# Optimization experiments

Hardware: AMD Instinct MI355X
Metric: run time of the kernel (lower is better)

## Reference

```python
import jax, jax.numpy as jnp
import numpy as np

L, H, N = 8192, 1024, 1024
MAX_PHASE = 6.283


def setup_inputs() -> dict:
    key = jax.random.key(0)
    ks = jax.random.split(key, 9)
    input_real = jax.random.uniform(ks[0], (L, H), dtype=jnp.float32)
    input_imag = jax.random.uniform(ks[1], (L, H), dtype=jnp.float32)
    # LRU parameter init (r_min=0, r_max=1, max_phase=6.283)
    u1 = jax.random.uniform(ks[2], (N,), dtype=jnp.float32)
    u2 = jax.random.uniform(ks[3], (N,), dtype=jnp.float32)
    nu_log = jnp.log(-0.5 * jnp.log(u1))
    theta_log = jnp.log(u2 * MAX_PHASE)
    B_real = jax.random.normal(ks[4], (N, H), dtype=jnp.float32) / np.float32(np.sqrt(2 * H))
    B_imag = jax.random.normal(ks[5], (N, H), dtype=jnp.float32) / np.float32(np.sqrt(2 * H))
    C_real = jax.random.normal(ks[6], (H, N), dtype=jnp.float32) / np.float32(np.sqrt(N))
    C_imag = jax.random.normal(ks[7], (H, N), dtype=jnp.float32) / np.float32(np.sqrt(N))
    D = jax.random.normal(ks[8], (H,), dtype=jnp.float32)
    diag_lambda = jnp.exp(jax.lax.complex(-jnp.exp(nu_log), jnp.exp(theta_log)))
    gamma_log = jnp.log(jnp.sqrt(1.0 - jnp.abs(diag_lambda) ** 2))
    return dict(input_real=input_real, input_imag=input_imag,
                nu_log=nu_log, theta_log=theta_log,
                B_real=B_real, B_imag=B_imag,
                C_real=C_real, C_imag=C_imag,
                D=D, gamma_log=gamma_log)


def _binop(e_i, e_j):
    a_i, bu_i = e_i
    a_j, bu_j = e_j
    return a_j * a_i, a_j * bu_i + bu_j


def _lru_forward(input_real, input_imag, nu_log, theta_log,
                 B_real, B_imag, C_real, C_imag, D, gamma_log):
    u = jax.lax.complex(input_real, input_imag)                      # (L, H) complex
    Lambda = jnp.exp(jax.lax.complex(-jnp.exp(nu_log), jnp.exp(theta_log)))  # (N,)
    # Faithful to source: exp(i * gamma_log), NOT exp(gamma_log)
    exp_gamma = jnp.exp(jax.lax.complex(jnp.zeros_like(gamma_log), gamma_log))  # (N,)
    B_norm = jax.lax.complex(B_real, B_imag) * exp_gamma[:, None]    # (N, H)
    Bu = jnp.einsum('lh,nh->ln', u, B_norm)                          # (L, N)
    Lambda_el = jnp.broadcast_to(Lambda[None, :], Bu.shape)          # (L, N)
    _, x = jax.lax.associative_scan(_binop, (Lambda_el, Bu))         # (L, N) states
    C = jax.lax.complex(C_real, C_imag)                              # (H, N)
    Dc = D.astype(C.dtype)                                           # (H,) complex
    y = jnp.real(jnp.einsum('ln,hn->lh', x, C)) + jnp.real(Dc[None, :] * u)
    return y                                                         # (L, H) float32


def reference(input_real, input_imag, nu_log, theta_log,
              B_real, B_imag, C_real, C_imag, D, gamma_log):
    return _lru_forward(input_real, input_imag, nu_log, theta_log,
                        B_real, B_imag, C_real, C_imag, D, gamma_log)
```

## Files before the change

### kernel.cpp

```cpp
#include <hip/hip_runtime.h>
#include <math.h>

#define L_SEQ 8192
#define H_DIM 1024
#define N_DIM 1024
#define K2    2048
#define NCHUNK 256
#define CHUNK 32

typedef unsigned short u16;
typedef __attribute__((ext_vector_type(8))) __bf16 bf16x8;
typedef __attribute__((ext_vector_type(4))) float  f32x4;

__device__ __forceinline__ u16 f2bf(float x) {
    unsigned int u = __float_as_uint(x);
    u = (u + 0x7fffu + ((u >> 16) & 1u)) >> 16;
    return (u16)u;
}
__device__ __forceinline__ float bf2f(u16 h) {
    return __uint_as_float(((unsigned int)h) << 16);
}

__device__ __forceinline__ void gload_lds16(const void* g, void* s) {
    __builtin_amdgcn_global_load_lds(
        (const __attribute__((address_space(1))) unsigned int*)g,
        (__attribute__((address_space(3))) unsigned int*)s, 16, 0, 0);
}

__global__ void pack_u(const float* __restrict__ R, const float* __restrict__ I,
                       u16* __restrict__ A) {
    size_t t = (size_t)blockIdx.x * 256 + threadIdx.x;
    size_t base = t * 4;
    int lrow = (int)(base >> 10);
    int h    = (int)(base & 1023);
    float4 r  = *reinterpret_cast<const float4*>(R + base);
    float4 im = *reinterpret_cast<const float4*>(I + base);
    u16* p0 = A + ((size_t)lrow << 11) + h;
    *reinterpret_cast<ushort4*>(p0) =
        make_ushort4(f2bf(r.x), f2bf(r.y), f2bf(r.z), f2bf(r.w));
    *reinterpret_cast<ushort4*>(p0 + 1024) =
        make_ushort4(f2bf(im.x), f2bf(im.y), f2bf(im.z), f2bf(im.w));
}

__global__ void bnorm_pack(const float* __restrict__ Br, const float* __restrict__ Bi,
                           const float* __restrict__ G, u16* __restrict__ Bp) {
    size_t t = (size_t)blockIdx.x * 256 + threadIdx.x;
    size_t base = t * 4;
    int n = (int)(base >> 10);
    int h = (int)(base & 1023);
    float g = G[n];
    float sg, cg;
    sincosf(g, &sg, &cg);
    float4 br = *reinterpret_cast<const float4*>(Br + base);
    float4 bi = *reinterpret_cast<const float4*>(Bi + base);
    float nr0 = br.x * cg - bi.x * sg, ni0 = br.x * sg + bi.x * cg;
    float nr1 = br.y * cg - bi.y * sg, ni1 = br.y * sg + bi.y * cg;
    float nr2 = br.z * cg - bi.z * sg, ni2 = br.z * sg + bi.z * cg;
    float nr3 = br.w * cg - bi.w * sg, ni3 = br.w * sg + bi.w * cg;
    u16* row0 = Bp + (size_t)n * K2;
    u16* row1 = Bp + (size_t)(N_DIM + n) * K2;
    *reinterpret_cast<ushort4*>(row0 + h) =
        make_ushort4(f2bf(nr0), f2bf(nr1), f2bf(nr2), f2bf(nr3));
    *reinterpret_cast<ushort4*>(row0 + 1024 + h) =
        make_ushort4(f2bf(-ni0), f2bf(-ni1), f2bf(-ni2), f2bf(-ni3));
    *reinterpret_cast<ushort4*>(row1 + h) =
        make_ushort4(f2bf(ni0), f2bf(ni1), f2bf(ni2), f2bf(ni3));
    *reinterpret_cast<ushort4*>(row1 + 1024 + h) =
        make_ushort4(f2bf(nr0), f2bf(nr1), f2bf(nr2), f2bf(nr3));
}

__global__ void pack_C(const float* __restrict__ Cr, const float* __restrict__ Ci,
                       u16* __restrict__ Cp) {
    size_t t = (size_t)blockIdx.x * 256 + threadIdx.x;
    size_t base = t * 4;
    int h = (int)(base >> 10);
    int n = (int)(base & 1023);
    float4 cr = *reinterpret_cast<const float4*>(Cr + base);
    float4 ci = *reinterpret_cast<const float4*>(Ci + base);
    u16* row = Cp + (size_t)h * K2;
    *reinterpret_cast<ushort4*>(row + n) =
        make_ushort4(f2bf(cr.x), f2bf(cr.y), f2bf(cr.z), f2bf(cr.w));
    *reinterpret_cast<ushort4*>(row + 1024 + n) =
        make_ushort4(f2bf(-ci.x), f2bf(-ci.y), f2bf(-ci.z), f2bf(-ci.w));
}

__global__ __launch_bounds__(512, 2) void gemm_pipe(
    const u16* __restrict__ A, const u16* __restrict__ B, int Klen, int lda,
    u16* __restrict__ OutB, int ldo) {
    constexpr int ABYTES = 256 * 128;
    constexpr int SLOT   = 2 * ABYTES;
    __shared__ __attribute__((aligned(128))) char lds[2 * SLOT];
    const int tid = threadIdx.x;
    const int l   = tid & 63;
    const int w   = tid >> 6;
    const int wm  = w >> 2;
    const int wn  = w & 3;
    const long bm = (long)blockIdx.x * 256;
    const long bn = (long)blockIdx.y * 256;

    f32x4 acc[8][4];
#pragma unroll
    for (int i = 0; i < 8; ++i)
#pragma unroll
        for (int j = 0; j < 4; ++j) acc[i][j] = (f32x4){0.f, 0.f, 0.f, 0.f};

    const int    lr        = tid >> 3;
    const int    swzcol    = (((tid & 7) ^ (lr & 7)) << 4);
    const size_t rowstride = (size_t)lda * 2;
    const size_t a_src0    = (size_t)(bm + lr) * rowstride + swzcol;
    const size_t b_src0    = (size_t)(bn + lr) * rowstride + swzcol;
    const char*  Agb       = (const char*)A;
    const char*  Bgb       = (const char*)B;
    const int nt = Klen / 64;

    auto STAGE_A = [&](int kt, int h) {
        if (kt >= nt) return;
        const size_t kofs = (size_t)kt * 128;
        char* d = lds + (kt & 1) * SLOT + h * 16384 + tid * 16;
#pragma unroll
        for (int j = 0; j < 2; ++j)
            gload_lds16(Agb + a_src0 + (size_t)(h * 128 + j * 64) * rowstride + kofs,
                        d + j * 8192);
    };
    auto STAGE_B = [&](int kt, int h) {
        if (kt >= nt) return;
        const size_t kofs = (size_t)kt * 128;
        char* d = lds + (kt & 1) * SLOT + ABYTES + h * 16384 + tid * 16;
#pragma unroll
        for (int j = 0; j < 2; ++j)
            gload_lds16(Bgb + b_src0 + (size_t)(h * 128 + j * 64) * rowstride + kofs,
                        d + j * 8192);
    };

    const int l15   = l & 15;
    const int lslot = l >> 4;

    auto READ_A = [&](bf16x8 (&af)[8], const char* lA, int kk) {
#pragma unroll
        for (int mi = 0; mi < 8; ++mi) {
            int r   = wm * 128 + mi * 16 + l15;
            int sl3 = ((kk << 2) | lslot) ^ (r & 7);
            af[mi]  = *reinterpret_cast<const bf16x8*>(lA + r * 128 + sl3 * 16);
        }
    };
    auto READ_B = [&](bf16x8 (&bg)[4], const char* lB, int kk) {
#pragma unroll
        for (int ni = 0; ni < 4; ++ni) {
            int r   = wn * 64 + ni * 16 + l15;
            int sl3 = ((kk << 2) | lslot) ^ (r & 7);
            bg[ni]  = *reinterpret_cast<const bf16x8*>(lB + r * 128 + sl3 * 16);
        }
    };
    auto MFMA_Q = [&](bf16x8 (&af)[8], bf16x8 (&bg)[4], int qn) {
        __builtin_amdgcn_s_setprio(1);
#pragma unroll
        for (int mi = 0; mi < 8; ++mi)
#pragma unroll
            for (int nj = 0; nj < 2; ++nj)
                acc[mi][qn * 2 + nj] = __builtin_amdgcn_mfma_f32_16x16x32_bf16(
                    af[mi], bg[qn * 2 + nj], acc[mi][qn * 2 + nj], 0, 0, 0);
        __builtin_amdgcn_s_setprio(0);
    };

#define SBAR  do { __builtin_amdgcn_sched_barrier(0);                        \
    __builtin_amdgcn_s_barrier();                                            \
    __builtin_amdgcn_sched_barrier(0); } while (0)
#define LGKM0 do { asm volatile("s_waitcnt lgkmcnt(0)" ::: "memory");        \
    __builtin_amdgcn_sched_barrier(0); } while (0)

    STAGE_A(0, 0); STAGE_B(0, 0); STAGE_A(0, 1); STAGE_B(0, 1);
    STAGE_A(1, 0); STAGE_B(1, 0);
    asm volatile("s_waitcnt vmcnt(4)" ::: "memory");
    SBAR;

    bf16x8 af0[8], af1[8], bg0[4], bg1[4];

    for (int t = 0; t < nt; ++t) {
        const char* lA = lds + (t & 1) * SLOT;
        const char* lB = lA + ABYTES;
        READ_A(af0, lA, 0);
        READ_B(bg0, lB, 0);
        STAGE_A(t + 1, 1);
        LGKM0;
        MFMA_Q(af0, bg0, 0);
        READ_A(af1, lA, 1);
        READ_B(bg1, lB, 1);
        STAGE_B(t + 1, 1);
        MFMA_Q(af0, bg0, 1);
        LGKM0;
        SBAR;
        STAGE_A(t + 2, 0);
        MFMA_Q(af1, bg1, 0);
        STAGE_B(t + 2, 0);
        MFMA_Q(af1, bg1, 1);
        if (t < nt - 2) asm volatile("s_waitcnt vmcnt(4)" ::: "memory");
        else            asm volatile("s_waitcnt vmcnt(0)" ::: "memory");
        SBAR;
    }
#undef SBAR
#undef LGKM0

#pragma unroll
    for (int mi = 0; mi < 8; ++mi) {
        const long row0 = bm + wm * 128 + mi * 16 + ((l >> 4) << 2);
#pragma unroll
        for (int ni = 0; ni < 4; ++ni) {
            const long col = bn + wn * 64 + ni * 16 + l15;
#pragma unroll
            for (int r = 0; r < 4; ++r)
                OutB[(size_t)(row0 + r) * ldo + col] = f2bf(acc[mi][ni][r]);
        }
    }
}

__global__ __launch_bounds__(256, 2) void gemm_small(
    const u16* __restrict__ A, const u16* __restrict__ B, int Klen, int lda,
    float* __restrict__ OutF, int ldo,
    const float* __restrict__ Dv, const float* __restrict__ Ur) {
    constexpr int ABYTES = 128 * 128;
    constexpr int SLOT   = 2 * ABYTES;
    __shared__ __attribute__((aligned(128))) char lds[2 * SLOT];
    const int tid = threadIdx.x;
    const int l   = tid & 63;
    const int w   = tid >> 6;
    const int wm  = w >> 1;
    const int wn  = w & 1;
    const long bm = (long)blockIdx.x * 128;
    const long bn = (long)blockIdx.y * 128;

    f32x4 acc[4][4];
#pragma unroll
    for (int i = 0; i < 4; ++i)
#pragma unroll
        for (int j = 0; j < 4; ++j) acc[i][j] = (f32x4){0.f, 0.f, 0.f, 0.f};

    const int    lr        = tid >> 3;
    const int    swzcol    = (((tid & 7) ^ (lr & 7)) << 4);
    const size_t rowstride = (size_t)lda * 2;
    const size_t a_src0    = (size_t)(bm + lr) * rowstride + swzcol;
    const size_t b_src0    = (size_t)(bn + lr) * rowstride + swzcol;
    const char*  Agb       = (const char*)A;
    const char*  Bgb       = (const char*)B;
    const int nt = Klen / 64;

    auto STAGE_A = [&](int kt, int h) {
        if (kt >= nt) return;
        const size_t kofs = (size_t)kt * 128;
        char* d = lds + (kt & 1) * SLOT + h * 8192 + tid * 16;
#pragma unroll
        for (int j = 0; j < 2; ++j)
            gload_lds16(Agb + a_src0 + (size_t)(h * 64 + j * 32) * rowstride + kofs,
                        d + j * 4096);
    };
    auto STAGE_B = [&](int kt, int h) {
        if (kt >= nt) return;
        const size_t kofs = (size_t)kt * 128;
        char* d = lds + (kt & 1) * SLOT + ABYTES + h * 8192 + tid * 16;
#pragma unroll
        for (int j = 0; j < 2; ++j)
            gload_lds16(Bgb + b_src0 + (size_t)(h * 64 + j * 32) * rowstride + kofs,
                        d + j * 4096);
    };

    const int l15   = l & 15;
    const int lslot = l >> 4;

    auto READ_A = [&](bf16x8 (&af)[4], const char* lA, int kk) {
#pragma unroll
        for (int mi = 0; mi < 4; ++mi) {
            int r   = wm * 64 + mi * 16 + l15;
            int sl3 = ((kk << 2) | lslot) ^ (r & 7);
            af[mi]  = *reinterpret_cast<const bf16x8*>(lA + r * 128 + sl3 * 16);
        }
    };
    auto READ_B = [&](bf16x8 (&bg)[4], const char* lB, int kk) {
#pragma unroll
        for (int ni = 0; ni < 4; ++ni) {
            int r   = wn * 64 + ni * 16 + l15;
            int sl3 = ((kk << 2) | lslot) ^ (r & 7);
            bg[ni]  = *reinterpret_cast<const bf16x8*>(lB + r * 128 + sl3 * 16);
        }
    };
    auto MFMA_Q = [&](bf16x8 (&af)[4], bf16x8 (&bg)[4], int qn) {
        __builtin_amdgcn_s_setprio(1);
#pragma unroll
        for (int mi = 0; mi < 4; ++mi)
#pragma unroll
            for (int nj = 0; nj < 2; ++nj)
                acc[mi][qn * 2 + nj] = __builtin_amdgcn_mfma_f32_16x16x32_bf16(
                    af[mi], bg[qn * 2 + nj], acc[mi][qn * 2 + nj], 0, 0, 0);
        __builtin_amdgcn_s_setprio(0);
    };

#define SBAR  do { __builtin_amdgcn_sched_barrier(0);                        \
    __builtin_amdgcn_s_barrier();                                            \
    __builtin_amdgcn_sched_barrier(0); } while (0)
#define LGKM0 do { asm volatile("s_waitcnt lgkmcnt(0)" ::: "memory");        \
    __builtin_amdgcn_sched_barrier(0); } while (0)

    STAGE_A(0, 0); STAGE_B(0, 0); STAGE_A(0, 1); STAGE_B(0, 1);
    STAGE_A(1, 0); STAGE_B(1, 0);
    asm volatile("s_waitcnt vmcnt(4)" ::: "memory");
    SBAR;

    bf16x8 af0[4], af1[4], bg0[4], bg1[4];

    for (int t = 0; t < nt; ++t) {
        const char* lA = lds + (t & 1) * SLOT;
        const char* lB = lA + ABYTES;
        READ_A(af0, lA, 0);
        READ_B(bg0, lB, 0);
        STAGE_A(t + 1, 1);
        LGKM0;
        MFMA_Q(af0, bg0, 0);
        READ_A(af1, lA, 1);
        READ_B(bg1, lB, 1);
        STAGE_B(t + 1, 1);
        MFMA_Q(af0, bg0, 1);
        LGKM0;
        SBAR;
        STAGE_A(t + 2, 0);
        MFMA_Q(af1, bg1, 0);
        STAGE_B(t + 2, 0);
        MFMA_Q(af1, bg1, 1);
        if (t < nt - 2) asm volatile("s_waitcnt vmcnt(4)" ::: "memory");
        else            asm volatile("s_waitcnt vmcnt(0)" ::: "memory");
        SBAR;
    }
#undef SBAR
#undef LGKM0

#pragma unroll
    for (int mi = 0; mi < 4; ++mi) {
        const long row0 = bm + wm * 64 + mi * 16 + ((l >> 4) << 2);
#pragma unroll
        for (int ni = 0; ni < 4; ++ni) {
            const long col = bn + wn * 64 + ni * 16 + l15;
            const float d = Dv[col];
#pragma unroll
            for (int r = 0; r < 4; ++r) {
                size_t o = (size_t)(row0 + r) * ldo + col;
                OutF[o] = acc[mi][ni][r] + d * Ur[o];
            }
        }
    }
}

__global__ void scan_sum(const u16* __restrict__ X,
                         const float* __restrict__ nu_log,
                         const float* __restrict__ theta_log,
                         float* __restrict__ bcr, float* __restrict__ bci) {
    int n0 = (blockIdx.y * 256 + threadIdx.x) * 2;
    int c  = blockIdx.x;
    float lr0, li0, lr1, li1;
    {
        float m0 = expf(-expf(nu_log[n0]));
        float t0 = expf(theta_log[n0]);
        float s0, c0; sincosf(t0, &s0, &c0);
        lr0 = m0 * c0; li0 = m0 * s0;
        float m1 = expf(-expf(nu_log[n0 + 1]));
        float t1 = expf(theta_log[n0 + 1]);
        float s1, c1; sincosf(t1, &s1, &c1);
        lr1 = m1 * c1; li1 = m1 * s1;
    }
    float sr0 = 0.f, si0 = 0.f, sr1 = 0.f, si1 = 0.f;
    size_t base = (size_t)c * CHUNK * K2 + n0;
    for (int j = 0; j < CHUNK; ++j) {
        size_t idx = base + (size_t)j * K2;
        unsigned int ru = *reinterpret_cast<const unsigned int*>(X + idx);
        unsigned int iu = *reinterpret_cast<const unsigned int*>(X + idx + 1024);
        float br0 = bf2f((u16)ru), br1 = bf2f((u16)(ru >> 16));
        float bi0 = bf2f((u16)iu), bi1 = bf2f((u16)(iu >> 16));
        float nr0 = lr0 * sr0 - li0 * si0 + br0;
        float ni0 = lr0 * si0 + li0 * sr0 + bi0;
        sr0 = nr0; si0 = ni0;
        float nr1 = lr1 * sr1 - li1 * si1 + br1;
        float ni1 = lr1 * si1 + li1 * sr1 + bi1;
        sr1 = nr1; si1 = ni1;
    }
    bcr[(size_t)n0 * NCHUNK + c] = sr0; bci[(size_t)n0 * NCHUNK + c] = si0;
    bcr[(size_t)(n0 + 1) * NCHUNK + c] = sr1; bci[(size_t)(n0 + 1) * NCHUNK + c] = si1;
}

__global__ void scan_carry(const float* __restrict__ bcr, const float* __restrict__ bci,
                           const float* __restrict__ nu_log,
                           const float* __restrict__ theta_log,
                           float* __restrict__ car, float* __restrict__ cai) {
    const int lane = threadIdx.x & 63;
    const int n    = blockIdx.x * 4 + (threadIdx.x >> 6);
    float mag = expf(-(float)CHUNK * expf(nu_log[n]));
    float ang = (float)CHUNK * expf(theta_log[n]);
    float sL, cL; sincosf(ang, &sL, &cL);
    const float Lr = mag * cL, Li = mag * sL;
    const size_t base = (size_t)n * NCHUNK + lane * 4;
    float4 br4 = *reinterpret_cast<const float4*>(bcr + base);
    float4 bi4 = *reinterpret_cast<const float4*>(bci + base);
    float br = br4.x, bi = bi4.x;
    { float tr = Lr * br - Li * bi + br4.y, ti = Lr * bi + Li * br + bi4.y; br = tr; bi = ti; }
    { float tr = Lr * br - Li * bi + br4.z, ti = Lr * bi + Li * br + bi4.z; br = tr; bi = ti; }
    { float tr = Lr * br - Li * bi + br4.w, ti = Lr * bi + Li * br + bi4.w; br = tr; bi = ti; }
    float L2r = Lr * Lr - Li * Li, L2i = 2.f * Lr * Li;
    float Ar = L2r * L2r - L2i * L2i, Ai = 2.f * L2r * L2i;
#pragma unroll
    for (int d = 1; d < 64; d <<= 1) {
        float pAr = __shfl_up(Ar, d);
        float pAi = __shfl_up(Ai, d);
        float pbr = __shfl_up(br, d);
        float pbi = __shfl_up(bi, d);
        if (lane >= d) {
            float nbr = Ar * pbr - Ai * pbi + br;
            float nbi = Ar * pbi + Ai * pbr + bi;
            float nAr = Ar * pAr - Ai * pAi;
            float nAi = Ar * pAi + Ai * pAr;
            br = nbr; bi = nbi; Ar = nAr; Ai = nAi;
        }
    }
    float sr = __shfl_up(br, 1);
    float si = __shfl_up(bi, 1);
    if (lane == 0) { sr = 0.f; si = 0.f; }
    float4 or4, oi4;
    or4.x = sr; oi4.x = si;
    { float tr = Lr * sr - Li * si + br4.x, ti = Lr * si + Li * sr + bi4.x; sr = tr; si = ti; }
    or4.y = sr; oi4.y = si;
    { float tr = Lr * sr - Li * si + br4.y, ti = Lr * si + Li * sr + bi4.y; sr = tr; si = ti; }
    or4.z = sr; oi4.z = si;
    { float tr = Lr * sr - Li * si + br4.z, ti = Lr * si + Li * sr + bi4.z; sr = tr; si = ti; }
    or4.w = sr; oi4.w = si;
    *reinterpret_cast<float4*>(car + base) = or4;
    *reinterpret_cast<float4*>(cai + base) = oi4;
}

__global__ void scan_apply(u16* __restrict__ X,
                           const float* __restrict__ nu_log,
                           const float* __restrict__ theta_log,
                           const float* __restrict__ car, const float* __restrict__ cai) {
    int n0 = (blockIdx.y * 256 + threadIdx.x) * 2;
    int c  = blockIdx.x;
    float lr0, li0, lr1, li1;
    {
        float m0 = expf(-expf(nu_log[n0]));
        float t0 = expf(theta_log[n0]);
        float s0, c0; sincosf(t0, &s0, &c0);
        lr0 = m0 * c0; li0 = m0 * s0;
        float m1 = expf(-expf(nu_log[n0 + 1]));
        float t1 = expf(theta_log[n0 + 1]);
        float s1, c1; sincosf(t1, &s1, &c1);
        lr1 = m1 * c1; li1 = m1 * s1;
    }
    float sr0 = car[(size_t)n0 * NCHUNK + c],       si0 = cai[(size_t)n0 * NCHUNK + c];
    float sr1 = car[(size_t)(n0 + 1) * NCHUNK + c], si1 = cai[(size_t)(n0 + 1) * NCHUNK + c];
    size_t base = (size_t)c * CHUNK * K2 + n0;
    for (int j = 0; j < CHUNK; ++j) {
        size_t idx = base + (size_t)j * K2;
        unsigned int ru = *reinterpret_cast<const unsigned int*>(X + idx);
        unsigned int iu = *reinterpret_cast<const unsigned int*>(X + idx + 1024);
        float br0 = bf2f((u16)ru), br1 = bf2f((u16)(ru >> 16));
        float bi0 = bf2f((u16)iu), bi1 = bf2f((u16)(iu >> 16));
        float nr0 = lr0 * sr0 - li0 * si0 + br0;
        float ni0 = lr0 * si0 + li0 * sr0 + bi0;
        sr0 = nr0; si0 = ni0;
        float nr1 = lr1 * sr1 - li1 * si1 + br1;
        float ni1 = lr1 * si1 + li1 * sr1 + bi1;
        sr1 = nr1; si1 = ni1;
        *reinterpret_cast<unsigned int*>(X + idx) =
            (unsigned int)f2bf(sr0) | ((unsigned int)f2bf(sr1) << 16);
        *reinterpret_cast<unsigned int*>(X + idx + 1024) =
            (unsigned int)f2bf(si0) | ((unsigned int)f2bf(si1) << 16);
    }
}

extern "C" void kernel_launch(void* const* d_in, const int* in_sizes, int n_in,
                              void* d_out, int out_size, void* d_ws, size_t ws_size,
                              hipStream_t stream) {
    (void)in_sizes; (void)n_in; (void)out_size; (void)ws_size;
    const float* input_real = (const float*)d_in[0];
    const float* input_imag = (const float*)d_in[1];
    const float* nu_log     = (const float*)d_in[2];
    const float* theta_log  = (const float*)d_in[3];
    const float* B_real     = (const float*)d_in[4];
    const float* B_imag     = (const float*)d_in[5];
    const float* C_real     = (const float*)d_in[6];
    const float* C_imag     = (const float*)d_in[7];
    const float* D          = (const float*)d_in[8];
    const float* gamma_log  = (const float*)d_in[9];
    float* y = (float*)d_out;

    char* ws = (char*)d_ws;
    u16* Ap   = (u16*)(ws + ((size_t)2 << 20));
    u16* Cp   = Ap;
    u16* Bp   = (u16*)(ws + ((size_t)34 << 20));
    float* bcr = (float*)(ws + ((size_t)34 << 20));
    float* bci = bcr + NCHUNK * N_DIM;
    float* car = bci + NCHUNK * N_DIM;
    float* cai = car + NCHUNK * N_DIM;
    u16* X    = (u16*)(ws + ((size_t)42 << 20));

    pack_u<<<(L_SEQ * H_DIM / 4) / 256, 256, 0, stream>>>(input_real, input_imag, Ap);
    bnorm_pack<<<(N_DIM * H_DIM / 4) / 256, 256, 0, stream>>>(B_real, B_imag, gamma_log, Bp);
    gemm_pipe<<<dim3(L_SEQ / 256, K2 / 256), 512, 0, stream>>>(
        Ap, Bp, K2, K2, X, K2);
    scan_sum<<<dim3(NCHUNK, N_DIM / 512), 256, 0, stream>>>(
        X, nu_log, theta_log, bcr, bci);
    scan_carry<<<N_DIM / 4, 256, 0, stream>>>(bcr, bci, nu_log, theta_log, car, cai);
    scan_apply<<<dim3(NCHUNK, N_DIM / 512), 256, 0, stream>>>(
        X, nu_log, theta_log, car, cai);
    pack_C<<<(H_DIM * N_DIM / 4) / 256, 256, 0, stream>>>(C_real, C_imag, Cp);
    gemm_small<<<dim3(L_SEQ / 128, H_DIM / 128), 256, 0, stream>>>(
        X, Cp, K2, K2, y, H_DIM, D, input_real);
}
```

Baseline: 153.7 us.

## Restructure big GEMM main loop into 8-wave quadrant ping-pong schedule

Rewrites the gemm_pipe main loop to process two K-tiles per iteration. Each wave reads quarter sub-tiles of A and B from LDS and issues MFMAs per quadrant, with barriers placed between quadrants. Global-to-LDS staging is interleaved between quadrant computations. The aim is finer overlap of LDS reads, global loads and MFMA work. The cost is many more barriers, and correctness depends on nt being even and on the new vmcnt accounting.

```diff
diff --git a/kernel.cpp b/kernel.cpp
--- a/kernel.cpp
+++ b/kernel.cpp
@@ -84,12 +84,12 @@
         make_ushort4(f2bf(-ci.x), f2bf(-ci.y), f2bf(-ci.z), f2bf(-ci.w));
 }
 
-__global__ __launch_bounds__(512, 2) void gemm_pipe(
+__global__ __launch_bounds__(512, 2) void gemm_pipe8(
     const u16* __restrict__ A, const u16* __restrict__ B, int Klen, int lda,
     u16* __restrict__ OutB, int ldo) {
-    constexpr int ABYTES = 256 * 128;
-    constexpr int SLOT   = 2 * ABYTES;
-    __shared__ __attribute__((aligned(128))) char lds[2 * SLOT];
+    constexpr int HALF = 16384;
+    constexpr int DBUF = 4 * HALF;
+    __shared__ __attribute__((aligned(128))) char lds[2 * DBUF];
     const int tid = threadIdx.x;
     const int l   = tid & 63;
     const int w   = tid >> 6;
@@ -116,7 +116,7 @@
     auto STAGE_A = [&](int kt, int h) {
         if (kt >= nt) return;
         const size_t kofs = (size_t)kt * 128;
-        char* d = lds + (kt & 1) * SLOT + h * 16384 + tid * 16;
+        char* d = lds + (kt & 1) * DBUF + h * HALF + tid * 16;
 #pragma unroll
         for (int j = 0; j < 2; ++j)
             gload_lds16(Agb + a_src0 + (size_t)(h * 128 + j * 64) * rowstride + kofs,
@@ -125,7 +125,7 @@
     auto STAGE_B = [&](int kt, int h) {
         if (kt >= nt) return;
         const size_t kofs = (size_t)kt * 128;
-        char* d = lds + (kt & 1) * SLOT + ABYTES + h * 16384 + tid * 16;
+        char* d = lds + (kt & 1) * DBUF + 2 * HALF + h * HALF + tid * 16;
 #pragma unroll
         for (int j = 0; j < 2; ++j)
             gload_lds16(Bgb + b_src0 + (size_t)(h * 128 + j * 64) * rowstride + kofs,
@@ -135,30 +135,42 @@
     const int l15   = l & 15;
     const int lslot = l >> 4;
 
-    auto READ_A = [&](bf16x8 (&af)[8], const char* lA, int kk) {
-#pragma unroll
-        for (int mi = 0; mi < 8; ++mi) {
-            int r   = wm * 128 + mi * 16 + l15;
-            int sl3 = ((kk << 2) | lslot) ^ (r & 7);
-            af[mi]  = *reinterpret_cast<const bf16x8*>(lA + r * 128 + sl3 * 16);
-        }
-    };
-    auto READ_B = [&](bf16x8 (&bg)[4], const char* lB, int kk) {
-#pragma unroll
-        for (int ni = 0; ni < 4; ++ni) {
-            int r   = wn * 64 + ni * 16 + l15;
-            int sl3 = ((kk << 2) | lslot) ^ (r & 7);
-            bg[ni]  = *reinterpret_cast<const bf16x8*>(lB + r * 128 + sl3 * 16);
-        }
-    };
-    auto MFMA_Q = [&](bf16x8 (&af)[8], bf16x8 (&bg)[4], int qn) {
+    auto READ_Asub = [&](bf16x8 (&af)[8], const char* db, int qa) {
+        const char* base = db + wm * HALF;
+#pragma unroll
+        for (int mi = 0; mi < 4; ++mi)
+#pragma unroll
+            for (int kk = 0; kk < 2; ++kk) {
+                int rw  = qa * 64 + mi * 16 + l15;
+                int sl3 = ((kk << 2) | lslot) ^ (rw & 7);
+                af[mi * 2 + kk] =
+                    *reinterpret_cast<const bf16x8*>(base + rw * 128 + sl3 * 16);
+            }
+    };
+    auto READ_Bsub = [&](bf16x8 (&bg)[4], const char* db, int qb) {
+        const char* base = db + 2 * HALF + (wn >> 1) * HALF;
+#pragma unroll
+        for (int nj = 0; nj < 2; ++nj)
+#pragma unroll
+            for (int kk = 0; kk < 2; ++kk) {
+                int rw  = (wn & 1) * 64 + qb * 32 + nj * 16 + l15;
+                int sl3 = ((kk << 2) | lslot) ^ (rw & 7);
+                bg[nj * 2 + kk] =
+                    *reinterpret_cast<const bf16x8*>(base + rw * 128 + sl3 * 16);
+            }
+    };
+    auto MFMA_Q = [&](bf16x8 (&af)[8], bf16x8 (&bg)[4], int qa, int qb) {
         __builtin_amdgcn_s_setprio(1);
 #pragma unroll
-        for (int mi = 0; mi < 8; ++mi)
+        for (int mi = 0; mi < 4; ++mi)
 #pragma unroll
             for (int nj = 0; nj < 2; ++nj)
-                acc[mi][qn * 2 + nj] = __builtin_amdgcn_mfma_f32_16x16x32_bf16(
-                    af[mi], bg[qn * 2 + nj], acc[mi][qn * 2 + nj], 0, 0, 0);
+#pragma unroll
+                for (int kk = 0; kk < 2; ++kk)
+                    acc[qa * 4 + mi][qb * 2 + nj] =
+                        __builtin_amdgcn_mfma_f32_16x16x32_bf16(
+                            af[mi * 2 + kk], bg[nj * 2 + kk],
+                            acc[qa * 4 + mi][qb * 2 + nj], 0, 0, 0);
         __builtin_amdgcn_s_setprio(0);
     };
 
@@ -168,33 +180,61 @@
 #define LGKM0 do { asm volatile("s_waitcnt lgkmcnt(0)" ::: "memory");        \
     __builtin_amdgcn_sched_barrier(0); } while (0)
 
-    STAGE_A(0, 0); STAGE_B(0, 0); STAGE_A(0, 1); STAGE_B(0, 1);
-    STAGE_A(1, 0); STAGE_B(1, 0);
+    STAGE_A(0, 0); STAGE_A(0, 1); STAGE_B(0, 0); STAGE_B(0, 1);
+    STAGE_A(1, 0); STAGE_A(1, 1);
     asm volatile("s_waitcnt vmcnt(4)" ::: "memory");
     SBAR;
 
-    bf16x8 af0[8], af1[8], bg0[4], bg1[4];
-
-    for (int t = 0; t < nt; ++t) {
-        const char* lA = lds + (t & 1) * SLOT;
-        const char* lB = lA + ABYTES;
-        READ_A(af0, lA, 0);
-        READ_B(bg0, lB, 0);
-        STAGE_A(t + 1, 1);
-        LGKM0;
-        MFMA_Q(af0, bg0, 0);
-        READ_A(af1, lA, 1);
-        READ_B(bg1, lB, 1);
-        STAGE_B(t + 1, 1);
-        MFMA_Q(af0, bg0, 1);
-        LGKM0;
-        SBAR;
-        STAGE_A(t + 2, 0);
-        MFMA_Q(af1, bg1, 0);
-        STAGE_B(t + 2, 0);
-        MFMA_Q(af1, bg1, 1);
-        if (t < nt - 2) asm volatile("s_waitcnt vmcnt(4)" ::: "memory");
-        else            asm volatile("s_waitcnt vmcnt(0)" ::: "memory");
+    bf16x8 afE[8], afO[8], bgE[4], bgO[4];
+    const int niter = nt / 2;
+
+    for (int i = 0; i < niter; ++i) {
+        const int t0 = 2 * i;
+        const int t1 = t0 + 1;
+        const char* d0 = lds + (t0 & 1) * DBUF;
+        const char* d1 = lds + (t1 & 1) * DBUF;
+        READ_Asub(afE, d0, 0);
+        READ_Bsub(bgE, d0, 0);
+        STAGE_B(t1, 0);
+        SBAR; LGKM0;
+        MFMA_Q(afE, bgE, 0, 0);
+        SBAR;
+        READ_Asub(afO, d0, 1);
+        STAGE_B(t1, 1);
+        SBAR; LGKM0;
+        MFMA_Q(afO, bgE, 1, 0);
+        SBAR;
+        READ_Bsub(bgO, d0, 1);
+        STAGE_A(t0 + 2, 0);
+        SBAR; LGKM0;
+        MFMA_Q(afO, bgO, 1, 1);
+        SBAR;
+        STAGE_A(t0 + 2, 1);
+        if (t0 + 2 < nt) asm volatile("s_waitcnt vmcnt(4)" ::: "memory");
+        else             asm volatile("s_waitcnt vmcnt(0)" ::: "memory");
+        SBAR;
+        MFMA_Q(afE, bgO, 0, 1);
+        SBAR;
+        READ_Asub(afE, d1, 0);
+        READ_Bsub(bgE, d1, 0);
+        STAGE_B(t0 + 2, 0);
+        SBAR; LGKM0;
+        MFMA_Q(afE, bgE, 0, 0);
+        SBAR;
+        READ_Asub(afO, d1, 1);
+        STAGE_B(t0 + 2, 1);
+        SBAR; LGKM0;
+        MFMA_Q(afO, bgE, 1, 0);
+        SBAR;
+        READ_Bsub(bgO, d1, 1);
+        STAGE_A(t1 + 2, 0);
+        SBAR; LGKM0;
+        MFMA_Q(afO, bgO, 1, 1);
+        SBAR;
+        STAGE_A(t1 + 2, 1);
+        if (i + 1 < niter) asm volatile("s_waitcnt vmcnt(4)" ::: "memory");
+        SBAR;
+        MFMA_Q(afE, bgO, 0, 1);
         SBAR;
     }
 #undef SBAR
@@ -497,7 +537,7 @@
 
     pack_u<<<(L_SEQ * H_DIM / 4) / 256, 256, 0, stream>>>(input_real, input_imag, Ap);
     bnorm_pack<<<(N_DIM * H_DIM / 4) / 256, 256, 0, stream>>>(B_real, B_imag, gamma_log, Bp);
-    gemm_pipe<<<dim3(L_SEQ / 256, K2 / 256), 512, 0, stream>>>(
+    gemm_pipe8<<<dim3(L_SEQ / 256, K2 / 256), 512, 0, stream>>>(
         Ap, Bp, K2, K2, X, K2);
     scan_sum<<<dim3(NCHUNK, N_DIM / 512), 256, 0, stream>>>(
         X, nu_log, theta_log, bcr, bci);
```

Result: slower. 157.9 us (+2.7%).
